# Kernel optimization log

Hardware: AMD Instinct MI355X
Metric: run time of the kernel (lower is better)

## Reference

```python
import jax, jax.numpy as jnp
import numpy as np

WPB = [4, 2, 2]          # words_per_block per scale
NH = 8                   # num_heads
DIM = 256                # feature dim (uniform, required by cross-scale einsums)
HD = DIM // NH           # per-head feature dim
W_PAR, W_PEER, W_KID = 0.5, 1.0, 2.0


def _linear(x, W):
    # torch nn.Linear (no bias): W is [out, in]
    return jnp.einsum('bhwi,oi->bhwo', x, W)


def _split_heads(y):
    # 'b h w (k f) -> b k h w f'
    b, H, Wd, D = y.shape
    return jnp.transpose(y.reshape(b, H, Wd, NH, D // NH), (0, 3, 1, 2, 4))


def _query(x, W):
    return _split_heads(_linear(x, W))


def _kv(x, W):
    # 'b h w (i k f) -> i b k h w f' with i=2
    y = _linear(x, W)
    b, H, Wd, D = y.shape
    y = y.reshape(b, H, Wd, 2, NH, D // (2 * NH))
    y = jnp.transpose(y, (3, 0, 4, 1, 2, 5))
    return y[0], y[1]


def _blocks(x, hb):
    # 'b k (h1 h2) (w1 w2) f -> b k h1 w1 (h2 w2) f'
    b, k, H, Wd, f = x.shape
    h1, w1 = H // hb, Wd // hb
    x = x.reshape(b, k, h1, hb, w1, hb, f)
    return jnp.transpose(x, (0, 1, 2, 4, 3, 5, 6)).reshape(b, k, h1, w1, hb * hb, f)


def _forward(xs, qpeer, kvpeer, qpar, kvpar, qkid, kvkid):
    n = len(WPB)
    outs = []
    for i in range(n):
        hb = WPB[i]
        hk = WPB[i + 1] if i < n - 1 else 0
        npar = 1 if i > 0 else 0
        scale = (hb + npar + hk) ** -0.5  # coupled scaling (decouple_scales=False)
        x = xs[i]
        b, Hi, Wi, _ = x.shape
        h1, w1 = Hi // hb, Wi // hb
        L = hb * hb  # queries per block
        attn, val, wts = [], [], []
        # --- peers ---
        qp = _blocks(_query(x, qpeer[i]), hb)
        kp, vp = _kv(x, kvpeer[i])
        kp, vp = _blocks(kp, hb), _blocks(vp, hb)
        attn.append(jnp.einsum('bkhwlf,bkhwmf->bkhwlm', qp, kp) * scale)
        val.append(jnp.broadcast_to(vp[:, :, :, :, None], (b, NH, h1, w1, L, L, HD)))
        wts.append(W_PEER * jnp.ones((L,), jnp.float32))
        # --- parents ---
        if i > 0:
            qpa = _blocks(_query(x, qpar[i - 1]), hb)
            kpa, vpa = _kv(xs[i - 1], kvpar[i - 1])  # [b,k,h1,w1,f]
            attn.append(jnp.einsum('bkhwlf,bkhwf->bkhwl', qpa, kpa)[..., None] * scale)
            val.append(jnp.broadcast_to(vpa[:, :, :, :, None, None, :], (b, NH, h1, w1, L, 1, HD)))
            wts.append(W_PAR * jnp.ones((1,), jnp.float32))
        # --- kids ---
        if i < n - 1:
            g = hk * hk
            qk = _query(x, qkid[i])               # [b,k,Hi,Wi,f]
            kk, vk = _kv(xs[i + 1], kvkid[i])
            kkb = _blocks(kk, hk)                  # [b,k,Hi,Wi,g,f]
            a = jnp.einsum('bkhwf,bkhwgf->bkhwg', qk, kkb) * scale
            a = jnp.transpose(a.reshape(b, NH, h1, hb, w1, hb, g), (0, 1, 2, 4, 3, 5, 6)).reshape(b, NH, h1, w1, L, g)
            attn.append(a)
            vkb = vk.reshape(b, NH, h1, hb, hk, w1, hb, hk, HD)
            vkb = jnp.transpose(vkb, (0, 1, 2, 5, 3, 6, 4, 7, 8)).reshape(b, NH, h1, w1, L, g, HD)
            val.append(vkb)
            wts.append(W_KID * jnp.ones((g,), jnp.float32))
        V = jnp.concatenate(val, axis=-2)          # [b,k,h1,w1,L,M,f]
        wvec = jnp.concatenate(wts)                # [M]
        A = jax.nn.softmax(jnp.concatenate(attn, axis=-1), axis=-1)
        A = wvec * A
        A = A / A.sum(-1, keepdims=True)
        # NOTE: faithful to the source einsum 'bkhwlm,bkhwlnf->bkhwlf' where m and n
        # are independently summed indices (attn row-sum times value sum over n).
        o = jnp.einsum('bkhwlm,bkhwlnf->bkhwlf', A, V)
        # 'b k h1 w1 (h2 w2) f -> b (h1 h2) (w1 w2) (k f)'
        o = jnp.transpose(o.reshape(b, NH, h1, w1, hb, hb, HD), (0, 2, 4, 3, 5, 1, 6)).reshape(b, Hi, Wi, NH * HD)
        outs.append(o)
    # forward returns ms_proj_drop(ms_slf_attn): projection output is discarded in the
    # source (ms_out is overwritten), and dropout is identity at p=0.
    return tuple(outs)


def setup_inputs() -> dict:
    key = jax.random.key(0)
    ks = iter(jax.random.split(key, 24))
    B = 8
    Hs = [16, 32, 64]
    d = {}
    for i in range(3):
        d[f'x{i}'] = jax.random.normal(next(ks), (B, Hs[i], Hs[i], DIM), jnp.float32)
    for i in range(3):
        d[f'qpeer_w{i}'] = 0.02 * jax.random.normal(next(ks), (DIM, DIM), jnp.float32)
        d[f'kvpeer_w{i}'] = 0.02 * jax.random.normal(next(ks), (2 * DIM, DIM), jnp.float32)
    for i in (1, 2):
        d[f'qpar_w{i}'] = 0.02 * jax.random.normal(next(ks), (DIM, DIM), jnp.float32)
        d[f'kvpar_w{i}'] = 0.02 * jax.random.normal(next(ks), (2 * DIM, DIM), jnp.float32)
    for i in (0, 1):
        d[f'qkid_w{i}'] = 0.02 * jax.random.normal(next(ks), (DIM, DIM), jnp.float32)
        d[f'kvkid_w{i}'] = 0.02 * jax.random.normal(next(ks), (2 * DIM, DIM), jnp.float32)
    return d


def reference(x0, x1, x2, qpeer_w0, qpeer_w1, qpeer_w2, kvpeer_w0, kvpeer_w1, kvpeer_w2,
              qpar_w1, qpar_w2, kvpar_w1, kvpar_w2, qkid_w0, qkid_w1, kvkid_w0, kvkid_w1):
    return _forward([x0, x1, x2],
                    [qpeer_w0, qpeer_w1, qpeer_w2],
                    [kvpeer_w0, kvpeer_w1, kvpeer_w2],
                    [qpar_w1, qpar_w2],
                    [kvpar_w1, kvpar_w2],
                    [qkid_w0, qkid_w1],
                    [kvkid_w0, kvkid_w1])
```

## Files before the change

### kernel.cpp

```cpp
#include <hip/hip_runtime.h>


constexpr int FD = 256;

typedef __attribute__((ext_vector_type(8))) short short8;
typedef __attribute__((ext_vector_type(4))) float floatx4;

__device__ inline unsigned short bf16bits(float f) {
  unsigned u = __builtin_bit_cast(unsigned, f);
  return (unsigned short)((u + 0x7fffu + ((u >> 16) & 1u)) >> 16);
}
__device__ inline ushort4 cvt4(float4 v) {
  ushort4 o;
  o.x = bf16bits(v.x); o.y = bf16bits(v.y);
  o.z = bf16bits(v.z); o.w = bf16bits(v.w);
  return o;
}

constexpr size_t OFF_S1 = 144 * 256;
constexpr size_t OFF_S2 = OFF_S1 + 2048 * 256;
constexpr size_t OFF_W = OFF_S2 + 8192 * 256;
constexpr size_t OFF_X0 = OFF_W + 7 * 65536;
constexpr size_t OFF_X1 = OFF_X0 + 2048 * 256;

__global__ __launch_bounds__(256) void prep(
    const float4* __restrict__ x0, const float4* __restrict__ x1,
    const float4* __restrict__ x2, const float* __restrict__ wp0,
    const float* __restrict__ wk0, const float* __restrict__ wp1,
    const float* __restrict__ wq1, const float* __restrict__ wk1,
    const float* __restrict__ wp2, const float* __restrict__ wq2,
    unsigned short* __restrict__ ws) {
  int blk = blockIdx.x;
  int t = threadIdx.x;
  if (blk < 2592) {
    const float4* x;
    unsigned short* S;
    unsigned short* xo = nullptr;
    int Hs, Ws, hb, row0;
    if (blk < 32) {
      x = x0; S = ws; xo = ws + OFF_X0; Hs = 4; Ws = 4; hb = 4; row0 = blk * 4;
    } else if (blk < 544) {
      x = x1; S = ws + OFF_S1; xo = ws + OFF_X1;
      Hs = 16; Ws = 16; hb = 2; row0 = (blk - 32) * 4;
    } else {
      x = x2; S = ws + OFF_S2; Hs = 32; Ws = 32; hb = 2; row0 = (blk - 544) * 4;
    }
    int c = t & 63;
    int row = row0 + (t >> 6);
    int bw = row % Ws;
    int t2 = row / Ws;
    int bh = t2 % Hs;
    int b = t2 / Hs;
    int W = Ws * hb;
    size_t base4 = (((size_t)b * Hs * hb + bh * hb) * W + bw * hb) * 64 + c;
    const float4* xb = x + base4;
    float4 s = {0.f, 0.f, 0.f, 0.f};
    for (int i = 0; i < hb; ++i)
      for (int j = 0; j < hb; ++j) {
        float4 v = xb[(size_t)(i * W + j) * 64];
        s.x += v.x; s.y += v.y; s.z += v.z; s.w += v.w;
        if (xo) *(ushort4*)(xo + (base4 + (size_t)(i * W + j) * 64) * 4) = cvt4(v);
      }
    *(ushort4*)(S + (size_t)row * FD + c * 4) = cvt4(s);
  } else {
    int wb = blk - 2592;
    int mat = wb >> 6;
    int row = (wb & 63) * 4 + (t >> 6);
    int c4 = (t & 63) * 4;
    const float* src;
    switch (mat) {
      case 0: src = wp0; break;
      case 1: src = wk0; break;
      case 2: src = wp1; break;
      case 3: src = wq1; break;
      case 4: src = wk1; break;
      case 5: src = wp2; break;
      default: src = wq2; break;
    }
    float4 v = *(const float4*)(src + (size_t)(256 + row) * FD + c4);
    *(ushort4*)(ws + OFF_W + (size_t)mat * 65536 + (size_t)row * FD + c4) =
        cvt4(v);
  }
}

#define MFMA(a, b, c) __builtin_amdgcn_mfma_f32_16x16x32_bf16(a, b, c, 0, 0, 0)

__global__ __launch_bounds__(256) void gemm(const unsigned short* __restrict__ ws,
                                            float* __restrict__ out0,
                                            float* __restrict__ out1,
                                            float* __restrict__ out2) {
  __shared__ float lds[4][16][17];
  int t = threadIdx.x;
  int l = t & 63;
  int wv = t >> 6;
  int c = l & 15, q = l >> 4;
  const short8* Wb = (const short8*)(ws + OFF_W);

  if (blockIdx.x < 1024) {
    int r0 = (blockIdx.x >> 2) * 32;
    int n0 = (blockIdx.x & 3) * 64;
    int n = n0 + wv * 16 + c;
    const short8* S2b = (const short8*)(ws + OFF_S2);
    const short8* X1b = (const short8*)(ws + OFF_X1);
    int cb0 = (r0 >> 10) * 256 + (((r0 >> 5) & 31) >> 1) * 16;
    const short8* aS1 = (const short8*)(ws + OFF_S1) + (size_t)(cb0 + c) * 32 + q;
    const short8* aX0 = (const short8*)(ws + OFF_X0) + (size_t)(cb0 + c) * 32 + q;
    const short8 *aS2[2], *aX1[2];
#pragma unroll
    for (int mt = 0; mt < 2; ++mt) {
      aS2[mt] = S2b + (size_t)(r0 + mt * 16 + c) * 32 + q;
      aX1[mt] = X1b + (size_t)(r0 + mt * 16 + c) * 32 + q;
    }
    const short8* bK1 = Wb + (size_t)4 * 8192 + (size_t)n * 32 + q;
    const short8* bP2 = Wb + (size_t)5 * 8192 + (size_t)n * 32 + q;
    const short8* bQ2 = Wb + (size_t)6 * 8192 + (size_t)n * 32 + q;
    const short8* bP1 = Wb + (size_t)2 * 8192 + (size_t)n * 32 + q;
    const short8* bQ1 = Wb + (size_t)3 * 8192 + (size_t)n * 32 + q;
    floatx4 accK[2] = {0, 0};
    floatx4 accC2[2] = {0, 0};
    floatx4 accC1 = {0, 0, 0, 0};
#pragma unroll 4
    for (int kk = 0; kk < 8; ++kk) {
      short8 k1 = bK1[kk * 4], p2 = bP2[kk * 4], q2 = bQ2[kk * 4];
      short8 p1 = bP1[kk * 4], q1 = bQ1[kk * 4];
      accC1 = MFMA(aS1[kk * 4], p1, accC1);
      accC1 = MFMA(aX0[kk * 4], q1, accC1);
#pragma unroll
      for (int mt = 0; mt < 2; ++mt) {
        short8 a = aS2[mt][kk * 4];
        accK[mt] = MFMA(a, k1, accK[mt]);
        accC2[mt] = MFMA(a, p2, accC2[mt]);
        accC2[mt] = MFMA(aX1[mt][kk * 4], q2, accC2[mt]);
      }
    }
#pragma unroll
    for (int r = 0; r < 4; ++r) lds[wv][4 * q + r][c] = accC1[r];
    __syncthreads();
#pragma unroll
    for (int mt = 0; mt < 2; ++mt)
#pragma unroll
      for (int r = 0; r < 4; ++r) {
        int rg = r0 + mt * 16 + 4 * q + r;
        int w = rg & 31;
        out1[(size_t)rg * FD + n] = accK[mt][r] + lds[wv][w >> 1][c];
        int b = rg >> 10, h = (rg >> 5) & 31;
        size_t o = ((size_t)b * 4096 + h * 128 + 2 * w) * FD + n;
        float v = accC2[mt][r];
        out2[o] = v;
        out2[o + FD] = v;
        out2[o + 16384] = v;
        out2[o + 16384 + FD] = v;
      }
  } else {
    int bid = blockIdx.x - 1024;
    int r0 = (bid >> 2) * 64;
    int n0 = (bid & 3) * 64;
    int n = n0 + wv * 16 + c;
    const short8* S1b = (const short8*)(ws + OFF_S1);
    const short8* aC = (const short8*)ws + (size_t)((r0 >> 4) + c) * 32 + q;
    const short8* bK = Wb + (size_t)1 * 8192 + (size_t)n * 32 + q;
    const short8* bP = Wb + (size_t)0 * 8192 + (size_t)n * 32 + q;
    const short8* aS[4];
#pragma unroll
    for (int mt = 0; mt < 4; ++mt)
      aS[mt] = S1b + (size_t)(r0 + mt * 16 + c) * 32 + q;
    floatx4 accK[4] = {0, 0, 0, 0};
    floatx4 accC = {0, 0, 0, 0};
#pragma unroll 4
    for (int kk = 0; kk < 8; ++kk) {
      short8 b0 = bK[kk * 4], b1 = bP[kk * 4];
      accC = MFMA(aC[kk * 4], b1, accC);
#pragma unroll
      for (int mt = 0; mt < 4; ++mt) accK[mt] = MFMA(aS[mt][kk * 4], b0, accK[mt]);
    }
    float s0 = __shfl(accC[0], c), s1 = __shfl(accC[1], c);
    float s2 = __shfl(accC[2], c), s3 = __shfl(accC[3], c);
    float cv = q == 0 ? s0 : q == 1 ? s1 : q == 2 ? s2 : s3;
#pragma unroll
    for (int mt = 0; mt < 4; ++mt)
#pragma unroll
      for (int r = 0; r < 4; ++r)
        out0[(size_t)(r0 + mt * 16 + 4 * q + r) * FD + n] = accK[mt][r] + cv;
  }
}

extern "C" void kernel_launch(void* const* d_in, const int* in_sizes, int n_in,
                              void* d_out, int out_size, void* d_ws,
                              size_t ws_size, hipStream_t stream) {
  const float* x0 = (const float*)d_in[0];
  const float* x1 = (const float*)d_in[1];
  const float* x2 = (const float*)d_in[2];

  const float *kvpeer0, *kvpeer1, *kvpeer2, *kvpar1, *kvpar2, *kvkid0, *kvkid1;
  if (n_in > 4 && in_sizes[4] == 2 * FD * FD) {
    kvpeer0 = (const float*)d_in[4];
    kvpeer1 = (const float*)d_in[6];
    kvpeer2 = (const float*)d_in[8];
    kvpar1 = (const float*)d_in[10];
    kvpar2 = (const float*)d_in[12];
    kvkid0 = (const float*)d_in[14];
    kvkid1 = (const float*)d_in[16];
  } else {
    kvpeer0 = (const float*)d_in[6];
    kvpeer1 = (const float*)d_in[7];
    kvpeer2 = (const float*)d_in[8];
    kvpar1 = (const float*)d_in[11];
    kvpar2 = (const float*)d_in[12];
    kvkid0 = (const float*)d_in[15];
    kvkid1 = (const float*)d_in[16];
  }

  unsigned short* ws = (unsigned short*)d_ws;
  float* out0 = (float*)d_out;
  float* out1 = out0 + (size_t)8 * 16 * 16 * FD;
  float* out2 = out1 + (size_t)8 * 32 * 32 * FD;

  prep<<<3040, 256, 0, stream>>>((const float4*)x0, (const float4*)x1,
                                 (const float4*)x2, kvpeer0, kvkid0, kvpeer1,
                                 kvpar1, kvkid1, kvpeer2, kvpar2, ws);
  gemm<<<1152, 256, 0, stream>>>(ws, out0, out1, out2);
}
```

Baseline: 181.0 us.

## Stage GEMM operand tiles through LDS and split the out2/out1 work into separate blocks

The GEMM kernel now cooperatively loads A and B tiles, in two K-halves, into a 48KB shared-memory buffer before running MFMAs out of LDS. Previously each wave read its operands directly from global memory. The scale-2 work (out2 replication) and the scale-1 work (out1 plus the kid term) are now handled by separate block ranges, with tiles of 64 rows by 32 columns. The grid doubles to 2304 blocks. This aims to improve operand reuse and memory coalescing and to spread work more evenly, at the cost of barriers, LDS traffic, some redundant reloads of the S2 tiles, and lower occupancy from the larger LDS footprint.

```diff
diff --git a/kernel.cpp b/kernel.cpp
--- a/kernel.cpp
+++ b/kernel.cpp
@@ -89,98 +89,231 @@
                                             float* __restrict__ out0,
                                             float* __restrict__ out1,
                                             float* __restrict__ out2) {
-  __shared__ float lds[4][16][17];
+  __shared__ __align__(16) char smem[49152];
   int t = threadIdx.x;
   int l = t & 63;
   int wv = t >> 6;
   int c = l & 15, q = l >> 4;
-  const short8* Wb = (const short8*)(ws + OFF_W);
+  const unsigned short* Wb = ws + OFF_W;
 
   if (blockIdx.x < 1024) {
-    int r0 = (blockIdx.x >> 2) * 32;
-    int n0 = (blockIdx.x & 3) * 64;
-    int n = n0 + wv * 16 + c;
-    const short8* S2b = (const short8*)(ws + OFF_S2);
-    const short8* X1b = (const short8*)(ws + OFF_X1);
+    int r0 = (int)(blockIdx.x >> 3) * 64;
+    int n0 = (int)(blockIdx.x & 7) * 32;
+    const unsigned short* gA0 = ws + OFF_S2;
+    const unsigned short* gA1 = ws + OFF_X1;
+    const unsigned short* gB0 = Wb + (size_t)5 * 65536;
+    const unsigned short* gB1 = Wb + (size_t)6 * 65536;
+    floatx4 acc[2] = {{0, 0, 0, 0}, {0, 0, 0, 0}};
+#pragma unroll
+    for (int kh = 0; kh < 2; ++kh) {
+      short8 v[12];
+#pragma unroll
+      for (int j = 0; j < 12; ++j) {
+        int ch = j * 256 + t;
+        const unsigned short* src;
+        if (j < 4) {
+          src = gA0 + (size_t)(r0 + (ch & 63)) * 256 + kh * 128 + (ch >> 6) * 8;
+        } else if (j < 8) {
+          int ca = ch - 1024;
+          src = gA1 + (size_t)(r0 + (ca & 63)) * 256 + kh * 128 + (ca >> 6) * 8;
+        } else if (j < 10) {
+          int cb = ch - 2048;
+          src = gB0 + (size_t)(n0 + (cb & 31)) * 256 + kh * 128 + (cb >> 5) * 8;
+        } else {
+          int cb = ch - 2560;
+          src = gB1 + (size_t)(n0 + (cb & 31)) * 256 + kh * 128 + (cb >> 5) * 8;
+        }
+        v[j] = *(const short8*)src;
+      }
+      __builtin_amdgcn_sched_barrier(0);
+#pragma unroll
+      for (int j = 0; j < 12; ++j)
+        *(short8*)(smem + (size_t)(j * 256 + t) * 16) = v[j];
+      __syncthreads();
+#pragma unroll
+      for (int kk = 0; kk < 4; ++kk) {
+        int kq = kk * 4 + q;
+        short8 a0 = *(const short8*)(smem + (size_t)(kq * 64 + wv * 16 + c) * 16);
+        short8 a1 =
+            *(const short8*)(smem + 16384 + (size_t)(kq * 64 + wv * 16 + c) * 16);
+#pragma unroll
+        for (int nt = 0; nt < 2; ++nt) {
+          short8 b0 =
+              *(const short8*)(smem + 32768 + (size_t)(kq * 32 + nt * 16 + c) * 16);
+          short8 b1 =
+              *(const short8*)(smem + 40960 + (size_t)(kq * 32 + nt * 16 + c) * 16);
+          acc[nt] = MFMA(a0, b0, acc[nt]);
+          acc[nt] = MFMA(a1, b1, acc[nt]);
+        }
+      }
+      __syncthreads();
+    }
+#pragma unroll
+    for (int nt = 0; nt < 2; ++nt) {
+      int n = n0 + nt * 16 + c;
+#pragma unroll
+      for (int r = 0; r < 4; ++r) {
+        int rg = r0 + wv * 16 + 4 * q + r;
+        int b = rg >> 10, h = (rg >> 5) & 31, w = rg & 31;
+        size_t o = ((size_t)b * 4096 + h * 128 + 2 * w) * FD + n;
+        float vv = acc[nt][r];
+        out2[o] = vv;
+        out2[o + FD] = vv;
+        out2[o + 16384] = vv;
+        out2[o + 16384 + FD] = vv;
+      }
+    }
+  } else if (blockIdx.x < 2048) {
+    int bid = blockIdx.x - 1024;
+    int r0 = (bid >> 3) * 64;
+    int n0 = (bid & 7) * 32;
     int cb0 = (r0 >> 10) * 256 + (((r0 >> 5) & 31) >> 1) * 16;
-    const short8* aS1 = (const short8*)(ws + OFF_S1) + (size_t)(cb0 + c) * 32 + q;
-    const short8* aX0 = (const short8*)(ws + OFF_X0) + (size_t)(cb0 + c) * 32 + q;
-    const short8 *aS2[2], *aX1[2];
-#pragma unroll
-    for (int mt = 0; mt < 2; ++mt) {
-      aS2[mt] = S2b + (size_t)(r0 + mt * 16 + c) * 32 + q;
-      aX1[mt] = X1b + (size_t)(r0 + mt * 16 + c) * 32 + q;
-    }
-    const short8* bK1 = Wb + (size_t)4 * 8192 + (size_t)n * 32 + q;
-    const short8* bP2 = Wb + (size_t)5 * 8192 + (size_t)n * 32 + q;
-    const short8* bQ2 = Wb + (size_t)6 * 8192 + (size_t)n * 32 + q;
-    const short8* bP1 = Wb + (size_t)2 * 8192 + (size_t)n * 32 + q;
-    const short8* bQ1 = Wb + (size_t)3 * 8192 + (size_t)n * 32 + q;
-    floatx4 accK[2] = {0, 0};
-    floatx4 accC2[2] = {0, 0};
-    floatx4 accC1 = {0, 0, 0, 0};
-#pragma unroll 4
-    for (int kk = 0; kk < 8; ++kk) {
-      short8 k1 = bK1[kk * 4], p2 = bP2[kk * 4], q2 = bQ2[kk * 4];
-      short8 p1 = bP1[kk * 4], q1 = bQ1[kk * 4];
-      accC1 = MFMA(aS1[kk * 4], p1, accC1);
-      accC1 = MFMA(aX0[kk * 4], q1, accC1);
-#pragma unroll
-      for (int mt = 0; mt < 2; ++mt) {
-        short8 a = aS2[mt][kk * 4];
-        accK[mt] = MFMA(a, k1, accK[mt]);
-        accC2[mt] = MFMA(a, p2, accC2[mt]);
-        accC2[mt] = MFMA(aX1[mt][kk * 4], q2, accC2[mt]);
-      }
-    }
-#pragma unroll
-    for (int r = 0; r < 4; ++r) lds[wv][4 * q + r][c] = accC1[r];
-    __syncthreads();
-#pragma unroll
-    for (int mt = 0; mt < 2; ++mt)
+    const unsigned short* gS2 = ws + OFF_S2;
+    const unsigned short* gS1 = ws + OFF_S1;
+    const unsigned short* gX0 = ws + OFF_X0;
+    const unsigned short* gBk = Wb + (size_t)4 * 65536;
+    const unsigned short* gBp = Wb + (size_t)2 * 65536;
+    const unsigned short* gBq = Wb + (size_t)3 * 65536;
+    floatx4 accK[2] = {{0, 0, 0, 0}, {0, 0, 0, 0}};
+    floatx4 accC[2] = {{0, 0, 0, 0}, {0, 0, 0, 0}};
+#pragma unroll
+    for (int kh = 0; kh < 2; ++kh) {
+      short8 v[12];
+#pragma unroll
+      for (int j = 0; j < 12; ++j) {
+        int ch = j * 256 + t;
+        const unsigned short* src;
+        if (j < 4) {
+          src = gS2 + (size_t)(r0 + (ch & 63)) * 256 + kh * 128 + (ch >> 6) * 8;
+        } else if (j < 5) {
+          int cs = ch - 1024;
+          src = gS1 + (size_t)(cb0 + (cs & 15)) * 256 + kh * 128 + (cs >> 4) * 8;
+        } else if (j < 6) {
+          int cs = ch - 1280;
+          src = gX0 + (size_t)(cb0 + (cs & 15)) * 256 + kh * 128 + (cs >> 4) * 8;
+        } else if (j < 8) {
+          int cb = ch - 1536;
+          src = gBk + (size_t)(n0 + (cb & 31)) * 256 + kh * 128 + (cb >> 5) * 8;
+        } else if (j < 10) {
+          int cb = ch - 2048;
+          src = gBp + (size_t)(n0 + (cb & 31)) * 256 + kh * 128 + (cb >> 5) * 8;
+        } else {
+          int cb = ch - 2560;
+          src = gBq + (size_t)(n0 + (cb & 31)) * 256 + kh * 128 + (cb >> 5) * 8;
+        }
+        v[j] = *(const short8*)src;
+      }
+      __builtin_amdgcn_sched_barrier(0);
+#pragma unroll
+      for (int j = 0; j < 12; ++j)
+        *(short8*)(smem + (size_t)(j * 256 + t) * 16) = v[j];
+      __syncthreads();
+#pragma unroll
+      for (int kk = 0; kk < 4; ++kk) {
+        int kq = kk * 4 + q;
+        short8 aS = *(const short8*)(smem + (size_t)(kq * 64 + wv * 16 + c) * 16);
+        short8 a1 = *(const short8*)(smem + 16384 + (size_t)(kq * 16 + c) * 16);
+        short8 ax = *(const short8*)(smem + 20480 + (size_t)(kq * 16 + c) * 16);
+#pragma unroll
+        for (int nt = 0; nt < 2; ++nt) {
+          short8 bk =
+              *(const short8*)(smem + 24576 + (size_t)(kq * 32 + nt * 16 + c) * 16);
+          short8 bp =
+              *(const short8*)(smem + 32768 + (size_t)(kq * 32 + nt * 16 + c) * 16);
+          short8 bq =
+              *(const short8*)(smem + 40960 + (size_t)(kq * 32 + nt * 16 + c) * 16);
+          accK[nt] = MFMA(aS, bk, accK[nt]);
+          accC[nt] = MFMA(a1, bp, accC[nt]);
+          accC[nt] = MFMA(ax, bq, accC[nt]);
+        }
+      }
+      __syncthreads();
+    }
+    int lsrc = ((wv & 1) * 2 + (q >> 1)) * 16 + c;
+#pragma unroll
+    for (int nt = 0; nt < 2; ++nt) {
+      int n = n0 + nt * 16 + c;
+      float s0 = __shfl(accC[nt][0], lsrc);
+      float s1 = __shfl(accC[nt][1], lsrc);
+      float s2 = __shfl(accC[nt][2], lsrc);
+      float s3 = __shfl(accC[nt][3], lsrc);
 #pragma unroll
       for (int r = 0; r < 4; ++r) {
-        int rg = r0 + mt * 16 + 4 * q + r;
-        int w = rg & 31;
-        out1[(size_t)rg * FD + n] = accK[mt][r] + lds[wv][w >> 1][c];
-        int b = rg >> 10, h = (rg >> 5) & 31;
-        size_t o = ((size_t)b * 4096 + h * 128 + 2 * w) * FD + n;
-        float v = accC2[mt][r];
-        out2[o] = v;
-        out2[o + FD] = v;
-        out2[o + 16384] = v;
-        out2[o + 16384 + FD] = v;
-      }
+        float cv;
+        if ((r >> 1) == 0)
+          cv = (q & 1) ? s2 : s0;
+        else
+          cv = (q & 1) ? s3 : s1;
+        int rg = r0 + wv * 16 + 4 * q + r;
+        out1[(size_t)rg * FD + n] = accK[nt][r] + cv;
+      }
+    }
   } else {
-    int bid = blockIdx.x - 1024;
-    int r0 = (bid >> 2) * 64;
-    int n0 = (bid & 3) * 64;
-    int n = n0 + wv * 16 + c;
-    const short8* S1b = (const short8*)(ws + OFF_S1);
-    const short8* aC = (const short8*)ws + (size_t)((r0 >> 4) + c) * 32 + q;
-    const short8* bK = Wb + (size_t)1 * 8192 + (size_t)n * 32 + q;
-    const short8* bP = Wb + (size_t)0 * 8192 + (size_t)n * 32 + q;
-    const short8* aS[4];
-#pragma unroll
-    for (int mt = 0; mt < 4; ++mt)
-      aS[mt] = S1b + (size_t)(r0 + mt * 16 + c) * 32 + q;
-    floatx4 accK[4] = {0, 0, 0, 0};
-    floatx4 accC = {0, 0, 0, 0};
-#pragma unroll 4
-    for (int kk = 0; kk < 8; ++kk) {
-      short8 b0 = bK[kk * 4], b1 = bP[kk * 4];
-      accC = MFMA(aC[kk * 4], b1, accC);
-#pragma unroll
-      for (int mt = 0; mt < 4; ++mt) accK[mt] = MFMA(aS[mt][kk * 4], b0, accK[mt]);
-    }
-    float s0 = __shfl(accC[0], c), s1 = __shfl(accC[1], c);
-    float s2 = __shfl(accC[2], c), s3 = __shfl(accC[3], c);
-    float cv = q == 0 ? s0 : q == 1 ? s1 : q == 2 ? s2 : s3;
-#pragma unroll
-    for (int mt = 0; mt < 4; ++mt)
+    int bid = blockIdx.x - 2048;
+    int r0 = (bid >> 3) * 64;
+    int n0 = (bid & 7) * 32;
+    int cr0 = r0 >> 4;
+    const unsigned short* gS1 = ws + OFF_S1;
+    const unsigned short* gS0 = ws;
+    const unsigned short* gBk = Wb + (size_t)1 * 65536;
+    const unsigned short* gBp = Wb + (size_t)0 * 65536;
+    floatx4 accK[2] = {{0, 0, 0, 0}, {0, 0, 0, 0}};
+    floatx4 accC[2] = {{0, 0, 0, 0}, {0, 0, 0, 0}};
+#pragma unroll
+    for (int kh = 0; kh < 2; ++kh) {
+      short8 v[9];
+#pragma unroll
+      for (int j = 0; j < 9; ++j) {
+        int ch = j * 256 + t;
+        const unsigned short* src;
+        if (j < 4) {
+          src = gS1 + (size_t)(r0 + (ch & 63)) * 256 + kh * 128 + (ch >> 6) * 8;
+        } else if (j < 5) {
+          int cs = ch - 1024;
+          src = gS0 + (size_t)(cr0 + (cs & 15)) * 256 + kh * 128 + (cs >> 4) * 8;
+        } else if (j < 7) {
+          int cb = ch - 1280;
+          src = gBk + (size_t)(n0 + (cb & 31)) * 256 + kh * 128 + (cb >> 5) * 8;
+        } else {
+          int cb = ch - 1792;
+          src = gBp + (size_t)(n0 + (cb & 31)) * 256 + kh * 128 + (cb >> 5) * 8;
+        }
+        v[j] = *(const short8*)src;
+      }
+      __builtin_amdgcn_sched_barrier(0);
+#pragma unroll
+      for (int j = 0; j < 9; ++j)
+        *(short8*)(smem + (size_t)(j * 256 + t) * 16) = v[j];
+      __syncthreads();
+#pragma unroll
+      for (int kk = 0; kk < 4; ++kk) {
+        int kq = kk * 4 + q;
+        short8 aS = *(const short8*)(smem + (size_t)(kq * 64 + wv * 16 + c) * 16);
+        short8 a0 = *(const short8*)(smem + 16384 + (size_t)(kq * 16 + c) * 16);
+#pragma unroll
+        for (int nt = 0; nt < 2; ++nt) {
+          short8 bk =
+              *(const short8*)(smem + 20480 + (size_t)(kq * 32 + nt * 16 + c) * 16);
+          short8 bp =
+              *(const short8*)(smem + 28672 + (size_t)(kq * 32 + nt * 16 + c) * 16);
+          accK[nt] = MFMA(aS, bk, accK[nt]);
+          accC[nt] = MFMA(a0, bp, accC[nt]);
+        }
+      }
+      __syncthreads();
+    }
+#pragma unroll
+    for (int nt = 0; nt < 2; ++nt) {
+      int n = n0 + nt * 16 + c;
+      float s0 = __shfl(accC[nt][0], c);
+      float s1 = __shfl(accC[nt][1], c);
+      float s2 = __shfl(accC[nt][2], c);
+      float s3 = __shfl(accC[nt][3], c);
+      float cv = q == 0 ? s0 : q == 1 ? s1 : q == 2 ? s2 : s3;
 #pragma unroll
       for (int r = 0; r < 4; ++r)
-        out0[(size_t)(r0 + mt * 16 + 4 * q + r) * FD + n] = accK[mt][r] + cv;
+        out0[(size_t)(r0 + wv * 16 + 4 * q + r) * FD + n] = accK[nt][r] + cv;
+    }
   }
 }
 
@@ -218,5 +351,5 @@
   prep<<<3040, 256, 0, stream>>>((const float4*)x0, (const float4*)x1,
                                  (const float4*)x2, kvpeer0, kvkid0, kvpeer1,
                                  kvpar1, kvkid1, kvpeer2, kvpar2, ws);
-  gemm<<<1152, 256, 0, stream>>>(ws, out0, out1, out2);
-}
+  gemm<<<2304, 256, 0, stream>>>(ws, out0, out1, out2);
+}
```

New measurement: 162.9 us. 1.11x faster.
